# Kernel tuning notes

Hardware: AMD Instinct MI355X
Metric: run time of the kernel (lower is better)

Reference implementation:

```python
import jax, jax.numpy as jnp
import numpy as np

K = 32  # neighbors per query point


def _gather_points(x, idx):
    # x: [B, N, D], idx: [B, M, k] -> [B, M, k, D]
    B, M, k = idx.shape
    D = x.shape[-1]
    flat = jnp.take_along_axis(x, idx.reshape(B, M * k, 1), axis=1)
    return flat.reshape(B, M, k, D)


def setup_inputs() -> dict:
    key = jax.random.key(0)
    k1, k2, k3, k4, k5 = jax.random.split(key, 5)
    B, N, M, Cin = 16, 4096, 1024, 64
    pos = jax.random.normal(k1, (B, N, 3), dtype=jnp.float32)
    features = jax.random.normal(k2, (B, N, Cin), dtype=jnp.float32)
    idx = jax.random.randint(k3, (B, M), 0, N, dtype=jnp.int64)
    # 1x1 conv2d MLP params: (Cin+3) -> 64 -> 128 (use_xyz adds 3 channels)
    W1 = jax.random.normal(k4, (Cin + 3, 64), dtype=jnp.float32) * (1.0 / np.sqrt(Cin + 3))
    b1 = jnp.zeros((64,), dtype=jnp.float32)
    W2 = jax.random.normal(k5, (64, 128), dtype=jnp.float32) * (1.0 / np.sqrt(64))
    b2 = jnp.zeros((128,), dtype=jnp.float32)
    return {"pos": pos, "features": features, "W1": W1, "b1": b1,
            "W2": W2, "b2": b2, "idx": idx}


def reference(pos, features, W1, b1, W2, b2, idx):
    # pos: [B,N,3], features: [B,N,C], idx: [B,M] query-point indices
    pos_q = jnp.take_along_axis(pos, idx[..., None], axis=1)  # [B,M,3]
    # squared-distance knn: [B,M,N]
    d2 = (jnp.sum(pos_q ** 2, -1, keepdims=True)
          + jnp.sum(pos ** 2, -1)[:, None, :]
          - 2.0 * jnp.einsum("bmd,bnd->bmn", pos_q, pos))
    _, nn_idx = jax.lax.top_k(-d2, K)  # [B,M,K] nearest neighbors
    grouped_pos = _gather_points(pos, nn_idx)          # [B,M,K,3]
    grouped_feat = _gather_points(features, nn_idx)    # [B,M,K,C]
    rel = grouped_pos - pos_q[:, :, None, :]           # recenter groups
    x = jnp.concatenate([rel, grouped_feat], axis=-1)  # [B,M,K,C+3] (use_xyz)
    # 1x1 conv2d MLP == per-point linear + ReLU on channel dim
    h = jax.nn.relu(jnp.einsum("bmkc,cd->bmkd", x, W1) + b1)
    h = jax.nn.relu(jnp.einsum("bmkc,cd->bmkd", h, W2) + b2)
    out = jnp.max(h, axis=-2)  # max over K neighbors -> [B,M,128]
    return (pos_q, out)
```

## Files before the change

kernel.cpp:

```cpp
#include <hip/hip_runtime.h>

#define NPTS  4096
#define MQ    1024
#define BATCH 16
#define KNN   32
#define CIN   64
#define H1D   64
#define H2D   128

typedef _Float16 half8 __attribute__((ext_vector_type(8)));
typedef float    floatx4 __attribute__((ext_vector_type(4)));

#define WS_NN_BYTES ((size_t)BATCH * MQ * KNN * 4)
#define W1F_HALVES  (3 * 4 * 64 * 8)
#define W2F_HALVES  (2 * 8 * 64 * 8)
#define WS_P4_OFF   (WS_NN_BYTES + (W1F_HALVES + W2F_HALVES) * 2)

__global__ __launch_bounds__(256) void wprep_kernel(
    const float* __restrict__ W1, const float* __restrict__ W2,
    const float* __restrict__ pos,
    _Float16* __restrict__ wout, float4* __restrict__ pos4)
{
    const int gid = blockIdx.x * 256 + threadIdx.x;
    if (gid < 768) {
        const int s = gid;
        const int kc = s >> 8, nt = (s >> 6) & 3, lane = s & 63;
        const int col = lane & 15, quad = lane >> 4;
        half8 ph;
#pragma unroll
        for (int j = 0; j < 8; ++j) {
            const int k = kc * 32 + quad * 8 + j;
            ph[j] = (k < 67) ? (_Float16)W1[k * H1D + nt * 16 + col] : (_Float16)0.0f;
        }
        *(half8*)(wout + (size_t)s * 8) = ph;
    } else if (gid < 1792) {
        const int s2 = gid - 768;
        const int kc2 = s2 >> 9, nt2 = (s2 >> 6) & 7, lane = s2 & 63;
        const int col = lane & 15, quad = lane >> 4;
        half8 ph;
#pragma unroll
        for (int j = 0; j < 8; ++j) {
            const int k = kc2 * 32 + quad * 8 + j;
            ph[j] = (_Float16)W2[k * H2D + nt2 * 16 + col];
        }
        *(half8*)(wout + (size_t)W1F_HALVES + (size_t)s2 * 8) = ph;
    } else {
        const int p = gid - 1792;
        if (p < BATCH * NPTS) {
            const float px = pos[p * 3 + 0], py = pos[p * 3 + 1], pz = pos[p * 3 + 2];
            float4 v;
            v.x = px; v.y = py; v.z = pz;
            v.w = __fadd_rn(__fadd_rn(__fmul_rn(px, px), __fmul_rn(py, py)),
                            __fmul_rn(pz, pz));
            pos4[p] = v;
        }
    }
}

__global__ __launch_bounds__(256, 4) void knn_kernel(
    const float4* __restrict__ pos4, const int* __restrict__ idx,
    float* __restrict__ pos_q, int* __restrict__ nn)
{
    const int bid = blockIdx.x;
    const int b   = bid >> 10;
    const int m   = bid & (MQ - 1);
    const int t   = threadIdx.x;
    const int wv  = t >> 6, lane = t & 63;

    __shared__ unsigned int hist[2048];
    __shared__ unsigned int wsum[4];
    __shared__ unsigned int sc[8];
    __shared__ unsigned int ckey[64];
    __shared__ int          cidx[64];
    __shared__ int          outidx[KNN];

    const float4* pb4 = pos4 + (size_t)b * NPTS;
    const int qn = idx[(size_t)b * MQ + m];
    const float4 qv = pb4[qn];
    const float qq = qv.w;

#pragma unroll
    for (int j = 0; j < 8; ++j) hist[t + 256 * j] = 0u;
    __syncthreads();

    unsigned int k[16];
#pragma unroll
    for (int i = 0; i < 16; ++i) {
        const float4 p = pb4[i * 256 + t];
        const float qp = __fadd_rn(__fadd_rn(__fmul_rn(qv.x, p.x), __fmul_rn(qv.y, p.y)),
                                   __fmul_rn(qv.z, p.z));
        const float d2 = __fsub_rn(__fadd_rn(qq, p.w), __fmul_rn(2.0f, qp));
        unsigned int u = __float_as_uint(d2);
        u = (u & 0x80000000u) ? ~u : (u | 0x80000000u);
        k[i] = u;
        atomicAdd(&hist[u >> 21], 1u);
    }
    __syncthreads();

    unsigned int prefix = 0u, rank = KNN - 1;
    int shift = 21, bcnt;
    for (int level = 0; level < 3; ++level) {
        const int nb = (level < 2) ? 11 : 10;
        const int g  = (1 << nb) >> 8;
        unsigned int cnt[8];
        unsigned int s = 0;
        for (int j = 0; j < g; ++j) { cnt[j] = hist[t * g + j]; s += cnt[j]; }
        unsigned int v = s;
#pragma unroll
        for (int off = 1; off < 64; off <<= 1) {
            const unsigned int o = __shfl_up(v, off);
            if (lane >= off) v += o;
        }
        if (lane == 63) wsum[wv] = v;
        __syncthreads();
        unsigned int woff = 0;
        for (int i = 0; i < wv; ++i) woff += wsum[i];
        const unsigned int incl = woff + v, excl = incl - s;
        if (rank >= excl && rank < incl) {
            unsigned int e = excl;
            for (int j = 0; j < g; ++j) {
                if (rank < e + cnt[j]) {
                    sc[0] = (prefix << nb) | (unsigned int)(t * g + j);
                    sc[1] = rank - e;
                    sc[2] = cnt[j];
                    break;
                }
                e += cnt[j];
            }
        }
        __syncthreads();
        prefix = sc[0];
        rank   = sc[1];
        bcnt   = (int)sc[2];
        if (level == 2 || bcnt <= 64) break;

        const int nshift = (level == 0) ? 10 : 0;
        const int nnb    = (level == 0) ? 11 : 10;
        const unsigned int nmask = (1u << nnb) - 1u;
        __syncthreads();
#pragma unroll
        for (int j = 0; j < 8; ++j) hist[t + 256 * j] = 0u;
        __syncthreads();
#pragma unroll
        for (int i = 0; i < 16; ++i) {
            const unsigned int u = k[i];
            if ((u >> (nshift + nnb)) == prefix)
                atomicAdd(&hist[(u >> nshift) & nmask], 1u);
        }
        shift = nshift;
        __syncthreads();
    }

    if (t == 0) { sc[3] = 0u; sc[4] = 0u; }
    __syncthreads();
#pragma unroll
    for (int i = 0; i < 16; ++i) {
        const unsigned int u = k[i];
        const unsigned int hp = (shift == 0) ? u : (u >> shift);
        if (hp < prefix) {
            outidx[atomicAdd(&sc[3], 1u)] = i * 256 + t;
        } else if (hp == prefix) {
            const unsigned int slot = atomicAdd(&sc[4], 1u);
            if (slot < 64u) { ckey[slot] = u; cidx[slot] = i * 256 + t; }
        }
    }
    __syncthreads();
    const int defcnt  = (int)sc[3];
    const int candcnt = min((int)sc[4], 64);

    if (wv == 0) {
        const unsigned int k_l = (lane < candcnt) ? ckey[lane] : 0xFFFFFFFFu;
        const int          i_l = (lane < candcnt) ? cidx[lane] : 0x7FFFFFFF;
        int rk = 0;
        for (int j = 0; j < candcnt; ++j) {
            const unsigned int kj = __shfl(k_l, j);
            const int          ij = __shfl(i_l, j);
            if (kj < k_l || (kj == k_l && ij < i_l)) ++rk;
        }
        if (lane < candcnt && rk <= (int)rank) outidx[defcnt + rk] = i_l;
    }
    __syncthreads();
    if (t < KNN) nn[(size_t)bid * KNN + t] = outidx[t];
    if (t == 0) {
        pos_q[(size_t)bid * 3 + 0] = qv.x;
        pos_q[(size_t)bid * 3 + 1] = qv.y;
        pos_q[(size_t)bid * 3 + 2] = qv.z;
    }
}

#define W1F_H 0
#define W2F_H 6144
#define XH_H  14336
#define SH_HALVES (XH_H + 4 * 3072)

__global__ __launch_bounds__(256) void mlp_kernel(
    const float* __restrict__ pos, const float* __restrict__ feat,
    const float* __restrict__ b1, const float* __restrict__ b2,
    const float* __restrict__ pos_q, const int* __restrict__ nn,
    const _Float16* __restrict__ wf, float* __restrict__ out)
{
    __shared__ _Float16 sh[SH_HALVES];
    const int t = threadIdx.x;
    const int w = t >> 6, lane = t & 63;
    const int col = lane & 15, quad = lane >> 4;
    const int qblk = blockIdx.x * 4;

    {
        const int4* src = (const int4*)wf;
        int4* dst = (int4*)sh;
#pragma unroll
        for (int r = 0; r < 7; ++r) dst[t + 256 * r] = src[t + 256 * r];
    }

    {
        const int r = t >> 1, h = t & 1;
        const int ql = r >> 5, kk = r & 31;
        const int q = qblk + ql, b = q >> 10;
        const int n = nn[(size_t)q * KNN + kk];
        const float* frow = feat + ((size_t)(b * NPTS + n)) * CIN;
        const float4* f4 = (const float4*)frow;
        const int mt = kk >> 4, lrow = kk & 15;
        const int base = XH_H + ql * 3072;
        if (h == 0) {
            float rel[3];
#pragma unroll
            for (int c = 0; c < 3; ++c)
                rel[c] = pos[(size_t)b * NPTS * 3 + n * 3 + c] - pos_q[(size_t)q * 3 + c];
            float fb[48];
#pragma unroll
            for (int ii = 0; ii < 12; ++ii) {
                const float4 v = f4[ii];
                fb[4*ii] = v.x; fb[4*ii+1] = v.y; fb[4*ii+2] = v.z; fb[4*ii+3] = v.w;
            }
#pragma unroll
            for (int cidx2 = 0; cidx2 < 6; ++cidx2) {
                half8 ph;
#pragma unroll
                for (int jj = 0; jj < 8; ++jj) {
                    const int c = cidx2 * 8 + jj;
                    ph[jj] = (_Float16)((c < 3) ? rel[c] : fb[c - 3]);
                }
                const int kc = cidx2 >> 2, qd = cidx2 & 3;
                *(half8*)&sh[base + ((kc * 2 + mt) * 64 + qd * 16 + lrow) * 8] = ph;
            }
        } else {
            float fb[20];
#pragma unroll
            for (int ii = 0; ii < 5; ++ii) {
                const float4 v = f4[11 + ii];
                fb[4*ii] = v.x; fb[4*ii+1] = v.y; fb[4*ii+2] = v.z; fb[4*ii+3] = v.w;
            }
#pragma unroll
            for (int cidx2 = 6; cidx2 < 12; ++cidx2) {
                half8 ph;
#pragma unroll
                for (int jj = 0; jj < 8; ++jj) {
                    const int c = cidx2 * 8 + jj;
                    ph[jj] = (_Float16)((c < 67) ? fb[c - 47] : 0.0f);
                }
                const int kc = cidx2 >> 2, qd = cidx2 & 3;
                *(half8*)&sh[base + ((kc * 2 + mt) * 64 + qd * 16 + lrow) * 8] = ph;
            }
        }
    }
    __syncthreads();

    const int q = qblk + w;
    const int wbase = XH_H + w * 3072;

    half8 af[3][2];
#pragma unroll
    for (int kc = 0; kc < 3; ++kc)
#pragma unroll
        for (int mt = 0; mt < 2; ++mt)
            af[kc][mt] = *(const half8*)&sh[wbase + ((kc * 2 + mt) * 64 + lane) * 8];

#pragma unroll
    for (int nt = 0; nt < 4; ++nt) {
        const float bv = b1[nt * 16 + col];
        floatx4 acc0 = {bv, bv, bv, bv}, acc1 = acc0;
#pragma unroll
        for (int kc = 0; kc < 3; ++kc) {
            const half8 bf = *(const half8*)&sh[W1F_H + ((kc * 4 + nt) * 64 + lane) * 8];
            acc0 = __builtin_amdgcn_mfma_f32_16x16x32_f16(af[kc][0], bf, acc0, 0, 0, 0);
            acc1 = __builtin_amdgcn_mfma_f32_16x16x32_f16(af[kc][1], bf, acc1, 0, 0, 0);
        }
        const int kc2 = nt >> 1;
        const int quad2 = (((nt & 1) * 16) + col) >> 3;
        const int j2 = col & 7;
#pragma unroll
        for (int mt = 0; mt < 2; ++mt) {
            const floatx4 a = mt ? acc1 : acc0;
#pragma unroll
            for (int reg = 0; reg < 4; ++reg) {
                const int row = quad * 4 + reg;
                sh[wbase + ((kc2 * 2 + mt) * 64 + quad2 * 16 + row) * 8 + j2] =
                    (_Float16)fmaxf(a[reg], 0.0f);
            }
        }
    }

    half8 a2[2][2];
#pragma unroll
    for (int kc2 = 0; kc2 < 2; ++kc2)
#pragma unroll
        for (int mt = 0; mt < 2; ++mt)
            a2[kc2][mt] = *(const half8*)&sh[wbase + ((kc2 * 2 + mt) * 64 + lane) * 8];

    float* oq = out + (size_t)q * H2D;
#pragma unroll
    for (int nt2 = 0; nt2 < 8; ++nt2) {
        const float bv = b2[nt2 * 16 + col];
        floatx4 acc0 = {bv, bv, bv, bv}, acc1 = acc0;
#pragma unroll
        for (int kc2 = 0; kc2 < 2; ++kc2) {
            const half8 bf = *(const half8*)&sh[W2F_H + ((kc2 * 8 + nt2) * 64 + lane) * 8];
            acc0 = __builtin_amdgcn_mfma_f32_16x16x32_f16(a2[kc2][0], bf, acc0, 0, 0, 0);
            acc1 = __builtin_amdgcn_mfma_f32_16x16x32_f16(a2[kc2][1], bf, acc1, 0, 0, 0);
        }
        float mm = fmaxf(fmaxf(fmaxf(acc0[0], acc0[1]), fmaxf(acc0[2], acc0[3])),
                         fmaxf(fmaxf(acc1[0], acc1[1]), fmaxf(acc1[2], acc1[3])));
        mm = fmaxf(mm, 0.0f);
        mm = fmaxf(mm, __shfl_xor(mm, 16));
        mm = fmaxf(mm, __shfl_xor(mm, 32));
        if (lane < 16) oq[nt2 * 16 + lane] = mm;
    }
}

extern "C" void kernel_launch(void* const* d_in, const int* in_sizes, int n_in,
                              void* d_out, int out_size, void* d_ws, size_t ws_size,
                              hipStream_t stream)
{
    const float* pos  = (const float*)d_in[0];
    const float* feat = (const float*)d_in[1];
    const float* W1   = (const float*)d_in[2];
    const float* b1   = (const float*)d_in[3];
    const float* W2   = (const float*)d_in[4];
    const float* b2   = (const float*)d_in[5];
    const int*   idx  = (const int*)d_in[6];

    float* pos_q = (float*)d_out;
    float* out   = (float*)d_out + (size_t)BATCH * MQ * 3;
    int*      nn = (int*)d_ws;
    _Float16* wf = (_Float16*)((char*)d_ws + WS_NN_BYTES);
    float4*   p4 = (float4*)((char*)d_ws + WS_P4_OFF);

    const int prep_threads = 1792 + BATCH * NPTS;
    wprep_kernel<<<(prep_threads + 255) / 256, 256, 0, stream>>>(W1, W2, pos, wf, p4);
    knn_kernel<<<BATCH * MQ, 256, 0, stream>>>(p4, idx, pos_q, nn);
    mlp_kernel<<<BATCH * MQ / 4, 256, 0, stream>>>(pos, feat, b1, b2,
                                                   pos_q, nn, wf, out);
}
```

Baseline: 204.9 us.

## Load MLP weights from global into registers and drop block-wide LDS staging

The MLP kernel no longer copies the packed fp16 W1/W2 fragments into shared memory. Each wave reads its weight fragments straight from global memory into registers, which removes the block-wide __syncthreads and shrinks shared memory so more blocks can fit per CU. Neighbor positions are now read as float4 from the prepacked pos4 buffer instead of three scalar loads. The kNN kernel also issues all 16 point loads up front before the distance math, to get more memory-level parallelism. The costs are higher register pressure, which the added launch bound of 4 blocks may force into spills, and repeated global/L2 reads of the weights by every wave.

```diff
diff --git a/kernel.cpp b/kernel.cpp
--- a/kernel.cpp
+++ b/kernel.cpp
@@ -83,13 +83,16 @@
     for (int j = 0; j < 8; ++j) hist[t + 256 * j] = 0u;
     __syncthreads();
 
+    float4 p[16];
+#pragma unroll
+    for (int i = 0; i < 16; ++i) p[i] = pb4[i * 256 + t];
+
     unsigned int k[16];
 #pragma unroll
     for (int i = 0; i < 16; ++i) {
-        const float4 p = pb4[i * 256 + t];
-        const float qp = __fadd_rn(__fadd_rn(__fmul_rn(qv.x, p.x), __fmul_rn(qv.y, p.y)),
-                                   __fmul_rn(qv.z, p.z));
-        const float d2 = __fsub_rn(__fadd_rn(qq, p.w), __fmul_rn(2.0f, qp));
+        const float qp = __fadd_rn(__fadd_rn(__fmul_rn(qv.x, p[i].x), __fmul_rn(qv.y, p[i].y)),
+                                   __fmul_rn(qv.z, p[i].z));
+        const float d2 = __fsub_rn(__fadd_rn(qq, p[i].w), __fmul_rn(2.0f, qp));
         unsigned int u = __float_as_uint(d2);
         u = (u & 0x80000000u) ? ~u : (u | 0x80000000u);
         k[i] = u;
@@ -188,85 +191,78 @@
     }
 }
 
-#define W1F_H 0
-#define W2F_H 6144
-#define XH_H  14336
-#define SH_HALVES (XH_H + 4 * 3072)
-
-__global__ __launch_bounds__(256) void mlp_kernel(
-    const float* __restrict__ pos, const float* __restrict__ feat,
+__global__ __launch_bounds__(256, 4) void mlp_kernel(
+    const float4* __restrict__ pos4, const float* __restrict__ feat,
     const float* __restrict__ b1, const float* __restrict__ b2,
     const float* __restrict__ pos_q, const int* __restrict__ nn,
     const _Float16* __restrict__ wf, float* __restrict__ out)
 {
-    __shared__ _Float16 sh[SH_HALVES];
+    __shared__ _Float16 sh[4 * 3072];
     const int t = threadIdx.x;
     const int w = t >> 6, lane = t & 63;
     const int col = lane & 15, quad = lane >> 4;
-    const int qblk = blockIdx.x * 4;
-
-    {
-        const int4* src = (const int4*)wf;
-        int4* dst = (int4*)sh;
-#pragma unroll
-        for (int r = 0; r < 7; ++r) dst[t + 256 * r] = src[t + 256 * r];
-    }
+    const int q = blockIdx.x * 4 + w;
+    const int b = q >> 10;
+    const int wbase = w * 3072;
 
     {
         const int r = t >> 1, h = t & 1;
-        const int ql = r >> 5, kk = r & 31;
-        const int q = qblk + ql, b = q >> 10;
+        const int kk = r & 31;
         const int n = nn[(size_t)q * KNN + kk];
-        const float* frow = feat + ((size_t)(b * NPTS + n)) * CIN;
-        const float4* f4 = (const float4*)frow;
+        const float4 pv = pos4[(size_t)b * NPTS + n];
+        const float4* f4 = (const float4*)(feat + ((size_t)b * NPTS + n) * CIN);
         const int mt = kk >> 4, lrow = kk & 15;
-        const int base = XH_H + ql * 3072;
         if (h == 0) {
+            float4 ff[12];
+#pragma unroll
+            for (int ii = 0; ii < 12; ++ii) ff[ii] = f4[ii];
             float rel[3];
-#pragma unroll
-            for (int c = 0; c < 3; ++c)
-                rel[c] = pos[(size_t)b * NPTS * 3 + n * 3 + c] - pos_q[(size_t)q * 3 + c];
-            float fb[48];
-#pragma unroll
-            for (int ii = 0; ii < 12; ++ii) {
-                const float4 v = f4[ii];
-                fb[4*ii] = v.x; fb[4*ii+1] = v.y; fb[4*ii+2] = v.z; fb[4*ii+3] = v.w;
-            }
-#pragma unroll
-            for (int cidx2 = 0; cidx2 < 6; ++cidx2) {
+            rel[0] = pv.x - pos_q[(size_t)q * 3 + 0];
+            rel[1] = pv.y - pos_q[(size_t)q * 3 + 1];
+            rel[2] = pv.z - pos_q[(size_t)q * 3 + 2];
+#pragma unroll
+            for (int ci = 0; ci < 6; ++ci) {
                 half8 ph;
 #pragma unroll
                 for (int jj = 0; jj < 8; ++jj) {
-                    const int c = cidx2 * 8 + jj;
-                    ph[jj] = (_Float16)((c < 3) ? rel[c] : fb[c - 3]);
+                    const int c = ci * 8 + jj;
+                    float v;
+                    if (c < 3) v = rel[c];
+                    else {
+                        const int fc = c - 3;
+                        const float4 vv = ff[fc >> 2];
+                        v = ((fc & 3) == 0) ? vv.x : ((fc & 3) == 1) ? vv.y
+                          : ((fc & 3) == 2) ? vv.z : vv.w;
+                    }
+                    ph[jj] = (_Float16)v;
                 }
-                const int kc = cidx2 >> 2, qd = cidx2 & 3;
-                *(half8*)&sh[base + ((kc * 2 + mt) * 64 + qd * 16 + lrow) * 8] = ph;
+                const int kc = ci >> 2, qd = ci & 3;
+                *(half8*)&sh[wbase + ((kc * 2 + mt) * 64 + qd * 16 + lrow) * 8] = ph;
             }
         } else {
-            float fb[20];
-#pragma unroll
-            for (int ii = 0; ii < 5; ++ii) {
-                const float4 v = f4[11 + ii];
-                fb[4*ii] = v.x; fb[4*ii+1] = v.y; fb[4*ii+2] = v.z; fb[4*ii+3] = v.w;
+            float4 ff[5];
+#pragma unroll
+            for (int ii = 0; ii < 5; ++ii) ff[ii] = f4[11 + ii];
+#pragma unroll
+            for (int ci = 6; ci < 12; ++ci) {
+                half8 ph;
+#pragma unroll
+                for (int jj = 0; jj < 8; ++jj) {
+                    const int c = ci * 8 + jj;
+                    float v = 0.0f;
+                    if (c < 67) {
+                        const int fc = c - 3;
+                        const float4 vv = ff[(fc >> 2) - 11];
+                        v = ((fc & 3) == 0) ? vv.x : ((fc & 3) == 1) ? vv.y
+                          : ((fc & 3) == 2) ? vv.z : vv.w;
+                    }
+                    ph[jj] = (_Float16)v;
+                }
+                const int kc = ci >> 2, qd = ci & 3;
+                *(half8*)&sh[wbase + ((kc * 2 + mt) * 64 + qd * 16 + lrow) * 8] = ph;
             }
-#pragma unroll
-            for (int cidx2 = 6; cidx2 < 12; ++cidx2) {
-                half8 ph;
-#pragma unroll
-                for (int jj = 0; jj < 8; ++jj) {
-                    const int c = cidx2 * 8 + jj;
-                    ph[jj] = (_Float16)((c < 67) ? fb[c - 47] : 0.0f);
-                }
-                const int kc = cidx2 >> 2, qd = cidx2 & 3;
-                *(half8*)&sh[base + ((kc * 2 + mt) * 64 + qd * 16 + lrow) * 8] = ph;
-            }
-        }
-    }
-    __syncthreads();
-
-    const int q = qblk + w;
-    const int wbase = XH_H + w * 3072;
+        }
+    }
 
     half8 af[3][2];
 #pragma unroll
@@ -274,6 +270,13 @@
 #pragma unroll
         for (int mt = 0; mt < 2; ++mt)
             af[kc][mt] = *(const half8*)&sh[wbase + ((kc * 2 + mt) * 64 + lane) * 8];
+
+    half8 w1f[3][4];
+#pragma unroll
+    for (int kc = 0; kc < 3; ++kc)
+#pragma unroll
+        for (int nt = 0; nt < 4; ++nt)
+            w1f[kc][nt] = *(const half8*)(wf + (size_t)((kc * 4 + nt) * 64 + lane) * 8);
 
 #pragma unroll
     for (int nt = 0; nt < 4; ++nt) {
@@ -281,9 +284,8 @@
         floatx4 acc0 = {bv, bv, bv, bv}, acc1 = acc0;
 #pragma unroll
         for (int kc = 0; kc < 3; ++kc) {
-            const half8 bf = *(const half8*)&sh[W1F_H + ((kc * 4 + nt) * 64 + lane) * 8];
-            acc0 = __builtin_amdgcn_mfma_f32_16x16x32_f16(af[kc][0], bf, acc0, 0, 0, 0);
-            acc1 = __builtin_amdgcn_mfma_f32_16x16x32_f16(af[kc][1], bf, acc1, 0, 0, 0);
+            acc0 = __builtin_amdgcn_mfma_f32_16x16x32_f16(af[kc][0], w1f[kc][nt], acc0, 0, 0, 0);
+            acc1 = __builtin_amdgcn_mfma_f32_16x16x32_f16(af[kc][1], w1f[kc][nt], acc1, 0, 0, 0);
         }
         const int kc2 = nt >> 1;
         const int quad2 = (((nt & 1) * 16) + col) >> 3;
@@ -307,6 +309,14 @@
         for (int mt = 0; mt < 2; ++mt)
             a2[kc2][mt] = *(const half8*)&sh[wbase + ((kc2 * 2 + mt) * 64 + lane) * 8];
 
+    half8 w2f[2][8];
+#pragma unroll
+    for (int kc2 = 0; kc2 < 2; ++kc2)
+#pragma unroll
+        for (int nt2 = 0; nt2 < 8; ++nt2)
+            w2f[kc2][nt2] = *(const half8*)(wf + (size_t)W1F_HALVES
+                                            + (size_t)((kc2 * 8 + nt2) * 64 + lane) * 8);
+
     float* oq = out + (size_t)q * H2D;
 #pragma unroll
     for (int nt2 = 0; nt2 < 8; ++nt2) {
@@ -314,9 +324,8 @@
         floatx4 acc0 = {bv, bv, bv, bv}, acc1 = acc0;
 #pragma unroll
         for (int kc2 = 0; kc2 < 2; ++kc2) {
-            const half8 bf = *(const half8*)&sh[W2F_H + ((kc2 * 8 + nt2) * 64 + lane) * 8];
-            acc0 = __builtin_amdgcn_mfma_f32_16x16x32_f16(a2[kc2][0], bf, acc0, 0, 0, 0);
-            acc1 = __builtin_amdgcn_mfma_f32_16x16x32_f16(a2[kc2][1], bf, acc1, 0, 0, 0);
+            acc0 = __builtin_amdgcn_mfma_f32_16x16x32_f16(a2[kc2][0], w2f[kc2][nt2], acc0, 0, 0, 0);
+            acc1 = __builtin_amdgcn_mfma_f32_16x16x32_f16(a2[kc2][1], w2f[kc2][nt2], acc1, 0, 0, 0);
         }
         float mm = fmaxf(fmaxf(fmaxf(acc0[0], acc0[1]), fmaxf(acc0[2], acc0[3])),
                          fmaxf(fmaxf(acc1[0], acc1[1]), fmaxf(acc1[2], acc1[3])));
@@ -348,6 +357,6 @@
     const int prep_threads = 1792 + BATCH * NPTS;
     wprep_kernel<<<(prep_threads + 255) / 256, 256, 0, stream>>>(W1, W2, pos, wf, p4);
     knn_kernel<<<BATCH * MQ, 256, 0, stream>>>(p4, idx, pos_q, nn);
-    mlp_kernel<<<BATCH * MQ / 4, 256, 0, stream>>>(pos, feat, b1, b2,
+    mlp_kernel<<<BATCH * MQ / 4, 256, 0, stream>>>(p4, feat, b1, b2,
                                                    pos_q, nn, wf, out);
 }
```

New measurement: 196.4 us. 1.04x faster.
